# Kernel optimization log

Hardware: AMD Instinct MI355X
Metric: run time of the kernel (lower is better)

Reference implementation:

```python
import jax, jax.numpy as jnp
import numpy as np

B, S, HID, NH, NS = 2, 1024, 2048, 16, 8
D = HID // NH  # head_dim = 128


def setup_inputs() -> dict:
    key = jax.random.key(0)
    ks = jax.random.split(key, 8)
    inv = 1.0 / np.sqrt(HID)
    return {
        "hidden_states": jax.random.normal(ks[0], (B, S, HID), jnp.float32),
        "Wq": jax.random.normal(ks[1], (HID, HID), jnp.float32) * inv,
        "Wk": jax.random.normal(ks[2], (HID, HID), jnp.float32) * inv,
        "Wv": jax.random.normal(ks[3], (HID, HID), jnp.float32) * inv,
        "Wo": jax.random.normal(ks[4], (HID, HID), jnp.float32) * inv,
        "splat_positions": jax.random.normal(ks[5], (NH, NS, D), jnp.float32) * 0.02,
        "splat_directions": jax.random.normal(ks[6], (NH, NS, D), jnp.float32) * 0.02,
        "splat_log_scales": jnp.full((NH, NS), np.log(0.8), jnp.float32),
        "splat_log_amplitudes": jnp.full((NH, NS), -np.log(float(NS)), jnp.float32),
        "directional_strength": jnp.float32(0.3),
        "gsa_strength": jnp.float32(-6.0),
    }


def _affinities(tokens, positions, directions, scales, dir_strength):
    # tokens [B,NH,S,D]; positions/directions [NH,NS,D]; scales [NH,NS]
    tok_sq = jnp.sum(tokens * tokens, axis=-1)                       # [B,NH,S]
    pos_sq = jnp.sum(positions * positions, axis=-1)                 # [NH,NS]
    tp = jnp.einsum('bhsd,hnd->bhsn', tokens, positions)             # [B,NH,S,NS]
    dist2 = tok_sq[..., None] - 2.0 * tp + pos_sq[None, :, None, :]
    dist2 = jnp.maximum(dist2, 0.0)
    # signed projection of (token - position) onto unit direction
    proj = (jnp.einsum('bhsd,hnd->bhsn', tokens, directions)
            - jnp.sum(positions * directions, axis=-1)[None, :, None, :])
    perp2 = jnp.maximum(dist2 - proj * proj, 0.0)
    inv2s2 = (0.5 / (scales * scales))[None, :, None, :]
    radial = jnp.exp(-dist2 * inv2s2)
    directional = jnp.exp(-perp2 * inv2s2)
    return (1.0 - dir_strength) * radial + dir_strength * directional


def reference(hidden_states, Wq, Wk, Wv, Wo, splat_positions, splat_directions,
              splat_log_scales, splat_log_amplitudes, directional_strength, gsa_strength):
    b, s, hid = hidden_states.shape

    def heads(x):  # [B,S,HID] -> [B,NH,S,D]
        return x.reshape(b, s, NH, D).transpose(0, 2, 1, 3)

    q = heads(hidden_states @ Wq)
    k = heads(hidden_states @ Wk)
    v = heads(hidden_states @ Wv)

    # --- standard (original) attention path ---
    scores = jnp.einsum('bhqd,bhkd->bhqk', q, k) / jnp.sqrt(jnp.float32(D))
    attn = jax.nn.softmax(scores, axis=-1)
    std = jnp.einsum('bhqk,bhkd->bhqd', attn, v)
    std = std.transpose(0, 2, 1, 3).reshape(b, s, hid) @ Wo

    # --- directional GSA path ---
    eps = 1e-12
    positions = splat_positions / (jnp.linalg.norm(splat_positions, axis=-1, keepdims=True) + eps)
    positions = positions * (np.sqrt(D) * 0.3)
    directions = splat_directions / (jnp.linalg.norm(splat_directions, axis=-1, keepdims=True) + eps)
    scales = jnp.clip(jnp.exp(splat_log_scales), 0.3, 1.2)
    amplitudes = jax.nn.softmax(splat_log_amplitudes, axis=-1)
    ds = jax.nn.sigmoid(directional_strength)

    qa = _affinities(q, positions, directions, scales, ds)  # [B,NH,S,NS]
    ka = _affinities(k, positions, directions, scales, ds)  # [B,NH,S,NS]
    w = jnp.einsum('bhqn,hn,bhkn->bhqk', qa, amplitudes, ka)
    w = w / (jnp.sum(w, axis=-1, keepdims=True) + 1e-8)
    dgsa = jnp.einsum('bhqk,bhkd->bhqd', w, v)
    dgsa = dgsa.transpose(0, 2, 1, 3).reshape(b, s, hid) @ Wo

    gsa = jax.nn.sigmoid(gsa_strength)
    blend = jnp.minimum(0.05, gsa * 0.1)
    return (1.0 - blend) * std + blend * dgsa
```

## Files before the change

kernel.cpp:

```cpp
#include <hip/hip_runtime.h>
#include <math.h>

typedef __attribute__((ext_vector_type(8))) short bf16x8;
typedef __attribute__((ext_vector_type(4))) float f32x4;
typedef unsigned short ushort_t;

#define SQRT_D 11.313708498984761f
#define INV_SQRT_D 0.08838834764831845f

__device__ __forceinline__ unsigned short f2b(float f) {
    unsigned u = __float_as_uint(f);
    unsigned r = (u + 0x7fffu + ((u >> 16) & 1u)) >> 16;
    return (unsigned short)r;
}
__device__ __forceinline__ float b2f(unsigned short h) {
    return __uint_as_float(((unsigned)h) << 16);
}

__device__ __forceinline__ void async_copy16(const void* g, void* l) {
    __builtin_amdgcn_global_load_lds((const __attribute__((address_space(1))) void*)g,
                                     (__attribute__((address_space(3))) void*)l, 16, 0, 0);
}

__global__ __launch_bounds__(256) void prep(
    const float* __restrict__ X, const float* __restrict__ W0,
    const float* __restrict__ W1, const float* __restrict__ W2,
    const float* __restrict__ W3, const float* __restrict__ sp,
    const float* __restrict__ sd, const float* __restrict__ ls,
    const float* __restrict__ la, ushort_t* __restrict__ Xbf,
    ushort_t* __restrict__ WT4, float* __restrict__ posn,
    float* __restrict__ dirn, float* __restrict__ pos_sq,
    float* __restrict__ pdv, float* __restrict__ iv2s2,
    float* __restrict__ amp) {
    __shared__ float t[32][33];
    const int z = blockIdx.z;
    if (z < 4) {
        const float* W = (z == 0) ? W0 : (z == 1) ? W1 : (z == 2) ? W2 : W3;
        ushort_t* WT = WT4 + (size_t)z * 4194304;
        int tx = threadIdx.x & 31, ty = threadIdx.x >> 5;
        int bn = blockIdx.x * 32, bk = blockIdx.y * 32;
#pragma unroll
        for (int i = 0; i < 4; ++i)
            t[ty + i * 8][tx] = W[(size_t)(bk + ty + i * 8) * 2048 + bn + tx];
        __syncthreads();
#pragma unroll
        for (int i = 0; i < 4; ++i)
            WT[(size_t)(bn + ty + i * 8) * 2048 + bk + tx] = f2b(t[tx][ty + i * 8]);
        return;
    }
    {
        int bi = blockIdx.y * 64 + blockIdx.x;
        int i = (bi * 256 + threadIdx.x) * 4;
        float4 v = *(const float4*)(X + i);
        ushort4 o;
        o.x = f2b(v.x); o.y = f2b(v.y); o.z = f2b(v.z); o.w = f2b(v.w);
        *(ushort4*)(Xbf + i) = o;
    }
    if (blockIdx.x == 0 && blockIdx.y == 0 && threadIdx.x < 128) {
        int i = threadIdx.x;
        const float* p = sp + (size_t)i * 128;
        const float* d = sd + (size_t)i * 128;
        float np_ = 0.f, nd_ = 0.f;
        for (int k = 0; k < 128; ++k) { np_ += p[k] * p[k]; nd_ += d[k] * d[k]; }
        np_ = sqrtf(np_); nd_ = sqrtf(nd_);
        const float sc = 3.394112549695428f;
        float rp = sc / (np_ + 1e-12f);
        float rd = 1.f / (nd_ + 1e-12f);
        float psq = 0.f, pd_ = 0.f;
        for (int k = 0; k < 128; ++k) {
            float pn = p[k] * rp;
            float dn = d[k] * rd;
            posn[(size_t)i * 128 + k] = pn;
            dirn[(size_t)i * 128 + k] = dn;
            psq += pn * pn;
            pd_ += pn * dn;
        }
        pos_sq[i] = psq;
        pdv[i] = pd_;
        float s = expf(ls[i]);
        s = fminf(fmaxf(s, 0.3f), 1.2f);
        iv2s2[i] = 0.5f / (s * s);
        if ((i & 7) == 0) {
            int h = i >> 3;
            float mx = -INFINITY;
            for (int n = 0; n < 8; ++n) mx = fmaxf(mx, la[h * 8 + n]);
            float e[8]; float ssum = 0.f;
            for (int n = 0; n < 8; ++n) { e[n] = expf(la[h * 8 + n] - mx); ssum += e[n]; }
            for (int n = 0; n < 8; ++n) amp[h * 8 + n] = e[n] / ssum;
        }
    }
}


__global__ __launch_bounds__(256) void gemm_qkv(const ushort_t* __restrict__ A,
                                                const ushort_t* __restrict__ WT4,
                                                ushort_t* __restrict__ Qb,
                                                ushort_t* __restrict__ Kb,
                                                ushort_t* __restrict__ Vb,
                                                ushort_t* __restrict__ Vt) {
    __shared__ ushort_t As0[128 * 32], As1[128 * 32];
    __shared__ ushort_t Bs0[128 * 32], Bs1[128 * 32];
    const int tid = threadIdx.x, lane = tid & 63, wave = tid >> 6;
    const int l15 = lane & 15, quad = lane >> 4;
    const int wm = (wave >> 1) * 64, wn = (wave & 1) * 64;
    const int bm = blockIdx.x * 128;
    const int by = blockIdx.y, which = by >> 4, bn = (by & 15) * 128;
    const ushort_t* BT = WT4 + (size_t)which * 4194304;
    f32x4 acc[4][4] = {};
    const int off0 = tid * 16;
    const int row0 = tid >> 2;
    const int c0 = (tid & 3) ^ ((row0 + (row0 >> 2)) & 3);
    const ushort_t* ga = A + (size_t)(bm + row0) * 2048 + c0 * 8;
    const ushort_t* gb = BT + (size_t)(bn + row0) * 2048 + c0 * 8;
    const int rsw = (l15 + (l15 >> 2)) & 3;
#define STAGEG(ABUF, BBUF, k_)                                                 \
    {                                                                          \
        async_copy16(ga + (k_), (char*)(ABUF) + off0);                         \
        async_copy16(ga + (size_t)64 * 2048 + (k_), (char*)(ABUF) + off0 + 4096); \
        async_copy16(gb + (k_), (char*)(BBUF) + off0);                         \
        async_copy16(gb + (size_t)64 * 2048 + (k_), (char*)(BBUF) + off0 + 4096); \
    }
#define COMPUTEG(ABUF, BBUF)                                                   \
    {                                                                          \
        bf16x8 af[4], bfr[4];                                                  \
        _Pragma("unroll") for (int i = 0; i < 4; ++i)                          \
            af[i] = *(const bf16x8*)((const char*)(ABUF) + (wm + i * 16 + l15) * 64 + ((quad ^ rsw) << 4)); \
        _Pragma("unroll") for (int j = 0; j < 4; ++j)                          \
            bfr[j] = *(const bf16x8*)((const char*)(BBUF) + (wn + j * 16 + l15) * 64 + ((quad ^ rsw) << 4)); \
        _Pragma("unroll") for (int i = 0; i < 4; ++i)                          \
            _Pragma("unroll") for (int j = 0; j < 4; ++j)                      \
                acc[i][j] = __builtin_amdgcn_mfma_f32_16x16x32_bf16(af[i], bfr[j], acc[i][j], 0, 0, 0); \
    }
    STAGEG(As0, Bs0, 0);
    for (int k0 = 0; k0 < 2048; k0 += 64) {
        __syncthreads();
        STAGEG(As1, Bs1, k0 + 32);
        COMPUTEG(As0, Bs0);
        __syncthreads();
        if (k0 + 64 < 2048) STAGEG(As0, Bs0, k0 + 64);
        COMPUTEG(As1, Bs1);
    }
#undef STAGEG
#undef COMPUTEG
    ushort_t* Cb = (which == 0) ? Qb : ((which == 1) ? Kb : Vb);
    const bool dot = (which == 2);
    const float oscale = (which == 0) ? INV_SQRT_D : 1.f;
#pragma unroll
    for (int i = 0; i < 4; ++i) {
#pragma unroll
        for (int j = 0; j < 4; ++j) {
            int m0 = bm + wm + i * 16 + quad * 4;
            int n = bn + wn + j * 16 + l15;
            int b = m0 >> 10, s0 = m0 & 1023, h = n >> 7, d = n & 127;
            ushort4 pack;
            unsigned short* pp = (unsigned short*)&pack;
#pragma unroll
            for (int r = 0; r < 4; ++r) {
                unsigned short bv = f2b(acc[i][j][r] * oscale);
                pp[r] = bv;
                Cb[((size_t)((b << 4) | h) * 1024 + (s0 + r)) * 128 + d] = bv;
            }
            if (dot) *(ushort4*)(Vt + ((size_t)((b << 4) | h) * 128 + d) * 1024 + s0) = pack;
        }
    }
}

__global__ __launch_bounds__(256) void gemm_out(const ushort_t* __restrict__ A,
                                                const ushort_t* __restrict__ BT,
                                                float* __restrict__ Cf) {
    __shared__ ushort_t As0[128 * 32], As1[128 * 32];
    __shared__ ushort_t Bs0[128 * 32], Bs1[128 * 32];
    const int tid = threadIdx.x, lane = tid & 63, wave = tid >> 6;
    const int l15 = lane & 15, quad = lane >> 4;
    const int wm = (wave >> 1) * 64, wn = (wave & 1) * 64;
    const int bm = blockIdx.x * 128, bn = blockIdx.y * 128;
    f32x4 acc[4][4] = {};
    const int off0 = tid * 16;
    const int row0 = tid >> 2;
    const int c0 = (tid & 3) ^ ((row0 + (row0 >> 2)) & 3);
    const ushort_t* ga = A + (size_t)(bm + row0) * 2048 + c0 * 8;
    const ushort_t* gb = BT + (size_t)(bn + row0) * 2048 + c0 * 8;
    const int rsw = (l15 + (l15 >> 2)) & 3;
#define STAGEO(ABUF, BBUF, k_)                                                 \
    {                                                                          \
        async_copy16(ga + (k_), (char*)(ABUF) + off0);                         \
        async_copy16(ga + (size_t)64 * 2048 + (k_), (char*)(ABUF) + off0 + 4096); \
        async_copy16(gb + (k_), (char*)(BBUF) + off0);                         \
        async_copy16(gb + (size_t)64 * 2048 + (k_), (char*)(BBUF) + off0 + 4096); \
    }
#define COMPUTEO(ABUF, BBUF)                                                   \
    {                                                                          \
        bf16x8 af[4], bfr[4];                                                  \
        _Pragma("unroll") for (int i = 0; i < 4; ++i)                          \
            af[i] = *(const bf16x8*)((const char*)(ABUF) + (wm + i * 16 + l15) * 64 + ((quad ^ rsw) << 4)); \
        _Pragma("unroll") for (int j = 0; j < 4; ++j)                          \
            bfr[j] = *(const bf16x8*)((const char*)(BBUF) + (wn + j * 16 + l15) * 64 + ((quad ^ rsw) << 4)); \
        _Pragma("unroll") for (int i = 0; i < 4; ++i)                          \
            _Pragma("unroll") for (int j = 0; j < 4; ++j)                      \
                acc[i][j] = __builtin_amdgcn_mfma_f32_16x16x32_bf16(af[i], bfr[j], acc[i][j], 0, 0, 0); \
    }
    STAGEO(As0, Bs0, 0);
    for (int k0 = 0; k0 < 2048; k0 += 64) {
        __syncthreads();
        STAGEO(As1, Bs1, k0 + 32);
        COMPUTEO(As0, Bs0);
        __syncthreads();
        if (k0 + 64 < 2048) STAGEO(As0, Bs0, k0 + 64);
        COMPUTEO(As1, Bs1);
    }
#undef STAGEO
#undef COMPUTEO
#pragma unroll
    for (int i = 0; i < 4; ++i)
#pragma unroll
        for (int j = 0; j < 4; ++j)
#pragma unroll
            for (int r = 0; r < 4; ++r) {
                int m = bm + wm + i * 16 + quad * 4 + r;
                int n = bn + wn + j * 16 + l15;
                Cf[(size_t)m * 2048 + n] = acc[i][j][r];
            }
}

__global__ __launch_bounds__(256) void affinity_q(
    const ushort_t* __restrict__ Q,
    const float* __restrict__ posn, const float* __restrict__ dirn,
    const float* __restrict__ pos_sq, const float* __restrict__ pdv,
    const float* __restrict__ iv2s2, const float* __restrict__ ds_in,
    float* __restrict__ qa) {
    int gid = blockIdx.x * 256 + threadIdx.x;
    int n = gid & 7;
    int t = gid >> 3;
    const ushort_t* T = Q + (size_t)t * 128;
    int h = (t >> 10) & 15;
    const float* P = posn + (size_t)(h * 8 + n) * 128;
    const float* Dr = dirn + (size_t)(h * 8 + n) * 128;
    float tsq = 0.f, tp = 0.f, td = 0.f;
#pragma unroll
    for (int d = 0; d < 128; d += 8) {
        uint4 raw = *(const uint4*)(T + d);
        float tv[8];
        tv[0] = __uint_as_float(raw.x << 16); tv[1] = __uint_as_float(raw.x & 0xffff0000u);
        tv[2] = __uint_as_float(raw.y << 16); tv[3] = __uint_as_float(raw.y & 0xffff0000u);
        tv[4] = __uint_as_float(raw.z << 16); tv[5] = __uint_as_float(raw.z & 0xffff0000u);
        tv[6] = __uint_as_float(raw.w << 16); tv[7] = __uint_as_float(raw.w & 0xffff0000u);
        float4 p0 = *(const float4*)(P + d), p1 = *(const float4*)(P + d + 4);
        float4 d0 = *(const float4*)(Dr + d), d1 = *(const float4*)(Dr + d + 4);
        tsq += tv[0]*tv[0]+tv[1]*tv[1]+tv[2]*tv[2]+tv[3]*tv[3]+tv[4]*tv[4]+tv[5]*tv[5]+tv[6]*tv[6]+tv[7]*tv[7];
        tp  += tv[0]*p0.x+tv[1]*p0.y+tv[2]*p0.z+tv[3]*p0.w+tv[4]*p1.x+tv[5]*p1.y+tv[6]*p1.z+tv[7]*p1.w;
        td  += tv[0]*d0.x+tv[1]*d0.y+tv[2]*d0.z+tv[3]*d0.w+tv[4]*d1.x+tv[5]*d1.y+tv[6]*d1.z+tv[7]*d1.w;
    }
    const float fs = SQRT_D;
    tsq *= fs * fs; tp *= fs; td *= fs;
    float dist2 = fmaxf(tsq - 2.f * tp + pos_sq[h * 8 + n], 0.f);
    float proj = td - pdv[h * 8 + n];
    float perp2 = fmaxf(dist2 - proj * proj, 0.f);
    float iv = iv2s2[h * 8 + n];
    float dsv = 1.f / (1.f + __expf(-ds_in[0]));
    float aff = (1.f - dsv) * __expf(-dist2 * iv) + dsv * __expf(-perp2 * iv);
    qa[(size_t)t * 8 + n] = aff;
}

__global__ __launch_bounds__(128) void kv_s1_part(
    const ushort_t* __restrict__ K, const ushort_t* __restrict__ V,
    const float* __restrict__ posn, const float* __restrict__ dirn,
    const float* __restrict__ pos_sq, const float* __restrict__ pdv,
    const float* __restrict__ iv2s2, const float* __restrict__ ds_in,
    float* __restrict__ KVp, float* __restrict__ S1p) {
    __shared__ float kas[64][8];
    int bh = blockIdx.x, sc = blockIdx.y;
    int tid = threadIdx.x;
    int h = bh & 15;
    if (tid < 64) {
        const ushort_t* T = K + ((size_t)bh * 1024 + sc * 64 + tid) * 128;
        float tsq = 0.f, tp[8] = {}, td[8] = {};
        for (int d = 0; d < 128; d += 4) {
            uint2 raw = *(const uint2*)(T + d);
            float t0 = __uint_as_float(raw.x << 16), t1 = __uint_as_float(raw.x & 0xffff0000u);
            float t2 = __uint_as_float(raw.y << 16), t3 = __uint_as_float(raw.y & 0xffff0000u);
            tsq += t0 * t0 + t1 * t1 + t2 * t2 + t3 * t3;
#pragma unroll
            for (int n = 0; n < 8; ++n) {
                const float* P = posn + (size_t)(h * 8 + n) * 128 + d;
                const float* Dr = dirn + (size_t)(h * 8 + n) * 128 + d;
                tp[n] += t0 * P[0] + t1 * P[1] + t2 * P[2] + t3 * P[3];
                td[n] += t0 * Dr[0] + t1 * Dr[1] + t2 * Dr[2] + t3 * Dr[3];
            }
        }
        float dsv = 1.f / (1.f + __expf(-ds_in[0]));
#pragma unroll
        for (int n = 0; n < 8; ++n) {
            float dist2 = fmaxf(tsq - 2.f * tp[n] + pos_sq[h * 8 + n], 0.f);
            float proj = td[n] - pdv[h * 8 + n];
            float perp2 = fmaxf(dist2 - proj * proj, 0.f);
            float iv = iv2s2[h * 8 + n];
            kas[tid][n] = (1.f - dsv) * __expf(-dist2 * iv) + dsv * __expf(-perp2 * iv);
        }
    }
    __syncthreads();
    int d = tid;
    const ushort_t* VB = V + ((size_t)bh * 1024 + sc * 64) * 128;
    float acc[8] = {};
#pragma unroll 4
    for (int s = 0; s < 64; ++s) {
        float vd = b2f(VB[(size_t)s * 128 + d]);
#pragma unroll
        for (int n = 0; n < 8; ++n) acc[n] += kas[s][n] * vd;
    }
#pragma unroll
    for (int n = 0; n < 8; ++n) KVp[(((size_t)bh * 8 + n) * 16 + sc) * 128 + d] = acc[n];
    __shared__ float s1p[128];
    {
        int n = d >> 4, chunk = d & 15;
        float p = 0.f;
        for (int s = chunk * 4; s < chunk * 4 + 4; ++s) p += kas[s][n];
        s1p[d] = p;
    }
    __syncthreads();
    if (d < 8) {
        float t = 0.f;
        for (int c = 0; c < 16; ++c) t += s1p[(d << 4) + c];
        S1p[((size_t)bh * 8 + d) * 16 + sc] = t;
    }
}

__global__ __launch_bounds__(256) void flash_blend(
    const ushort_t* __restrict__ Qg, const ushort_t* __restrict__ Kg,
    const ushort_t* __restrict__ Vtg,
    const float* __restrict__ qa, const float* __restrict__ amp,
    const float* __restrict__ S1p, const float* __restrict__ KVp,
    const float* __restrict__ gstr, ushort_t* __restrict__ blended) {
    __shared__ ushort_t Ks0[64 * 128], Ks1[64 * 128];
    __shared__ ushort_t Vt0[128 * 64], Vt1[128 * 64];
    __shared__ ushort_t Ps[4][16 * 72];
    __shared__ float KVs[8 * 128];
    __shared__ float S1s[8];
    const int tid = threadIdx.x, lane = tid & 63, wave = tid >> 6;
    const int l15 = lane & 15, quad = lane >> 4;
    const int bh = blockIdx.y, qt = blockIdx.x;

    const ushort_t* Qrow = Qg + ((size_t)(bh * 1024 + qt * 64 + wave * 16 + l15)) * 128 + quad * 8;
    bf16x8 aq[4];
#pragma unroll
    for (int k4 = 0; k4 < 4; ++k4) aq[k4] = *(const bf16x8*)(Qrow + k4 * 32);

    {
        int n = tid >> 5, d = (tid & 31) * 4;
        f32x4 kv = {};
#pragma unroll
        for (int sc = 0; sc < 16; ++sc)
            kv += *(const f32x4*)(KVp + (((size_t)bh * 8 + n) * 16 + sc) * 128 + d);
        *(f32x4*)(KVs + tid * 4) = kv;
    }
    if (tid < 8) {
        float s = 0.f;
#pragma unroll
        for (int sc = 0; sc < 16; ++sc) s += S1p[((size_t)bh * 8 + tid) * 16 + sc];
        S1s[tid] = s;
    }

    const ushort_t* Kbase = Kg + (size_t)bh * 131072;
    const ushort_t* Vbase = Vtg + (size_t)bh * 131072;

#define STAGE(KBUF, VBUF, kt_)                                                        \
    {                                                                                 \
        _Pragma("unroll") for (int i_ = 0; i_ < 4; ++i_) {                            \
            int off_ = tid * 16 + i_ * 4096;                                          \
            int kr_ = off_ >> 8, kp_ = (off_ >> 4) & 15;                              \
            async_copy16(Kbase + (size_t)(kt_)*8192 + kr_ * 128 + ((kp_ ^ (kr_ & 15)) << 3), \
                         (char*)(KBUF) + off_);                                       \
            int vd_ = off_ >> 7, vp_ = (off_ >> 4) & 7;                               \
            async_copy16(Vbase + (size_t)vd_ * 1024 + (kt_)*64 + ((vp_ ^ (vd_ & 7)) << 3), \
                         (char*)(VBUF) + off_);                                       \
        }                                                                             \
    }
#define FLASH_STEP(KBUF, VBUF)                                                        \
    {                                                                                 \
        f32x4 sc[4] = {};                                                             \
        _Pragma("unroll") for (int k4 = 0; k4 < 4; ++k4) {                            \
            _Pragma("unroll") for (int t = 0; t < 4; ++t) {                           \
                bf16x8 bk = *(const bf16x8*)((const char*)(KBUF) +                    \
                                             ((t * 16 + l15) << 8) + (((k4 * 4 + quad) ^ l15) << 4)); \
                sc[t] = __builtin_amdgcn_mfma_f32_16x16x32_bf16(aq[k4], bk, sc[t], 0, 0, 0); \
            }                                                                         \
        }                                                                             \
        _Pragma("unroll") for (int t = 0; t < 4; ++t) {                               \
            _Pragma("unroll") for (int r = 0; r < 4; ++r) {                           \
                float p = __expf(sc[t][r]);                                           \
                l_i[r] += p;                                                          \
                Pw[(quad * 4 + r) * 72 + t * 16 + l15] = f2b(p);                      \
            }                                                                         \
        }                                                                             \
        bf16x8 ap0 = *(const bf16x8*)((const char*)Pw + (l15 * 72 + quad * 8) * 2);   \
        bf16x8 ap1 = *(const bf16x8*)((const char*)Pw + (l15 * 72 + 32 + quad * 8) * 2); \
        _Pragma("unroll") for (int j = 0; j < 8; ++j) {                               \
            bf16x8 bv0 = *(const bf16x8*)((const char*)(VBUF) +                       \
                                          ((j * 16 + l15) << 7) + (((quad) ^ (l15 & 7)) << 4)); \
            bf16x8 bv1 = *(const bf16x8*)((const char*)(VBUF) +                       \
                                          ((j * 16 + l15) << 7) + (((4 + quad) ^ (l15 & 7)) << 4)); \
            o[j] = __builtin_amdgcn_mfma_f32_16x16x32_bf16(ap0, bv0, o[j], 0, 0, 0);  \
            o[j] = __builtin_amdgcn_mfma_f32_16x16x32_bf16(ap1, bv1, o[j], 0, 0, 0);  \
        }                                                                             \
    }

    STAGE(Ks0, Vt0, 0);

    f32x4 o[8] = {};
    float l_i[4] = {};
    ushort_t* Pw = &Ps[wave][0];

    for (int kt = 0; kt < 16; kt += 2) {
        __syncthreads();
        STAGE(Ks1, Vt1, kt + 1);
        FLASH_STEP(Ks0, Vt0);
        __syncthreads();
        if (kt + 2 < 16) STAGE(Ks0, Vt0, kt + 2);
        FLASH_STEP(Ks1, Vt1);
    }
#undef STAGE
#undef FLASH_STEP
#pragma unroll
    for (int r = 0; r < 4; ++r) {
        float l = l_i[r];
        l += __shfl_xor(l, 1);
        l += __shfl_xor(l, 2);
        l += __shfl_xor(l, 4);
        l += __shfl_xor(l, 8);
        l_i[r] = l;
    }
    float gsa = 1.f / (1.f + __expf(-gstr[0]));
    float blend = fminf(0.05f, gsa * 0.1f);
    int b = bh >> 4, h = bh & 15;
#pragma unroll
    for (int r = 0; r < 4; ++r) {
        int q = qt * 64 + wave * 16 + quad * 4 + r;
        const float* qaRow = qa + ((size_t)bh * 1024 + q) * 8;
        float qam[8], Z = 0.f;
#pragma unroll
        for (int n = 0; n < 8; ++n) {
            qam[n] = qaRow[n] * amp[h * 8 + n];
            Z += qam[n] * S1s[n];
        }
        float invZ = 1.f / (Z + 1e-8f);
        float invl = 1.f / l_i[r];
        ushort_t* outp = blended + ((size_t)(b * 1024 + q)) * 2048 + h * 128;
#pragma unroll
        for (int j = 0; j < 8; ++j) {
            int d = j * 16 + l15;
            float dg = 0.f;
#pragma unroll
            for (int n = 0; n < 8; ++n) dg += qam[n] * KVs[n * 128 + d];
            float v = (1.f - blend) * (o[j][r] * invl) + blend * (dg * invZ);
            outp[d] = f2b(v);
        }
    }
}

extern "C" void kernel_launch(void* const* d_in, const int* in_sizes, int n_in,
                              void* d_out, int out_size, void* d_ws, size_t ws_size,
                              hipStream_t stream) {
    const float* X = (const float*)d_in[0];
    const float* Wq = (const float*)d_in[1];
    const float* Wk = (const float*)d_in[2];
    const float* Wv = (const float*)d_in[3];
    const float* Wo = (const float*)d_in[4];
    const float* sp = (const float*)d_in[5];
    const float* sd = (const float*)d_in[6];
    const float* ls = (const float*)d_in[7];
    const float* la = (const float*)d_in[8];
    const float* dstr = (const float*)d_in[9];
    const float* gstr = (const float*)d_in[10];

    char* base = (char*)d_ws;
    ushort_t* WT4 = (ushort_t*)base;      base += 33554432;
    ushort_t* Xbf = (ushort_t*)base;      base += 8388608;
    ushort_t* blended = Xbf;
    ushort_t* Qbf = (ushort_t*)base;      base += 8388608;
    ushort_t* Kbf = (ushort_t*)base;      base += 8388608;
    ushort_t* Vbf = (ushort_t*)base;      base += 8388608;
    ushort_t* Vtb = (ushort_t*)base;      base += 8388608;
    float* qaw = (float*)base;            base += 1048576;
    float* posn = (float*)base;           base += 65536;
    float* dirn = (float*)base;           base += 65536;
    float* pos_sq = (float*)base;         base += 512;
    float* pdv = (float*)base;            base += 512;
    float* iv2s2 = (float*)base;          base += 512;
    float* ampw = (float*)base;           base += 512;
    float* S1p = (float*)base;            base += 16384;
    float* KVp = (float*)base;            base += 2097152;

    prep<<<dim3(64, 64, 5), 256, 0, stream>>>(X, Wq, Wk, Wv, Wo, sp, sd, ls, la,
                                              Xbf, WT4, posn, dirn, pos_sq, pdv, iv2s2, ampw);
    gemm_qkv<<<dim3(16, 48), 256, 0, stream>>>(Xbf, WT4, Qbf, Kbf, Vbf, Vtb);
    affinity_q<<<1024, 256, 0, stream>>>(Qbf, posn, dirn, pos_sq, pdv, iv2s2, dstr, qaw);
    kv_s1_part<<<dim3(32, 16), 128, 0, stream>>>(Kbf, Vbf, posn, dirn, pos_sq, pdv, iv2s2,
                                                 dstr, KVp, S1p);
    flash_blend<<<dim3(16, 32), 256, 0, stream>>>(Qbf, Kbf, Vtb, qaw, ampw, S1p, KVp,
                                                  gstr, blended);
    gemm_out<<<dim3(16, 16), 256, 0, stream>>>(blended, WT4 + 12582912, (float*)d_out);
}
```

Before: 328.7 us.

## Read K/V directly from global in flash kernel, halve block size

Removes the double-buffered LDS staging of K and Vt tiles with async copies and barriers; each wave now loads MFMA operands for K and Vt straight from global memory, relying on L1/L2 caching. The query tile shrinks to 32 rows with 128-thread blocks, doubling the grid to 1024 blocks. This cuts LDS usage and synchronization to raise occupancy, at the cost of redundant, less-coalesced global reads of K/V shared across waves.

```diff
diff --git a/kernel.cpp b/kernel.cpp
--- a/kernel.cpp
+++ b/kernel.cpp
@@ -324,33 +324,35 @@
     }
 }
 
-__global__ __launch_bounds__(256) void flash_blend(
+__global__ __launch_bounds__(128) void flash_blend(
     const ushort_t* __restrict__ Qg, const ushort_t* __restrict__ Kg,
     const ushort_t* __restrict__ Vtg,
     const float* __restrict__ qa, const float* __restrict__ amp,
     const float* __restrict__ S1p, const float* __restrict__ KVp,
     const float* __restrict__ gstr, ushort_t* __restrict__ blended) {
-    __shared__ ushort_t Ks0[64 * 128], Ks1[64 * 128];
-    __shared__ ushort_t Vt0[128 * 64], Vt1[128 * 64];
-    __shared__ ushort_t Ps[4][16 * 72];
+    __shared__ ushort_t Ps[2][16 * 72];
     __shared__ float KVs[8 * 128];
     __shared__ float S1s[8];
     const int tid = threadIdx.x, lane = tid & 63, wave = tid >> 6;
     const int l15 = lane & 15, quad = lane >> 4;
     const int bh = blockIdx.y, qt = blockIdx.x;
 
-    const ushort_t* Qrow = Qg + ((size_t)(bh * 1024 + qt * 64 + wave * 16 + l15)) * 128 + quad * 8;
+    const ushort_t* Qrow = Qg + ((size_t)(bh * 1024 + qt * 32 + wave * 16 + l15)) * 128 + quad * 8;
     bf16x8 aq[4];
 #pragma unroll
     for (int k4 = 0; k4 < 4; ++k4) aq[k4] = *(const bf16x8*)(Qrow + k4 * 32);
 
     {
-        int n = tid >> 5, d = (tid & 31) * 4;
-        f32x4 kv = {};
-#pragma unroll
-        for (int sc = 0; sc < 16; ++sc)
-            kv += *(const f32x4*)(KVp + (((size_t)bh * 8 + n) * 16 + sc) * 128 + d);
-        *(f32x4*)(KVs + tid * 4) = kv;
+        int n = tid >> 4, d0 = (tid & 15) * 8;
+        f32x4 kv0 = {}, kv1 = {};
+#pragma unroll
+        for (int sc = 0; sc < 16; ++sc) {
+            const float* src = KVp + (((size_t)bh * 8 + n) * 16 + sc) * 128 + d0;
+            kv0 += *(const f32x4*)(src);
+            kv1 += *(const f32x4*)(src + 4);
+        }
+        *(f32x4*)(KVs + n * 128 + d0) = kv0;
+        *(f32x4*)(KVs + n * 128 + d0 + 4) = kv1;
     }
     if (tid < 8) {
         float s = 0.f;
@@ -361,64 +363,43 @@
 
     const ushort_t* Kbase = Kg + (size_t)bh * 131072;
     const ushort_t* Vbase = Vtg + (size_t)bh * 131072;
-
-#define STAGE(KBUF, VBUF, kt_)                                                        \
-    {                                                                                 \
-        _Pragma("unroll") for (int i_ = 0; i_ < 4; ++i_) {                            \
-            int off_ = tid * 16 + i_ * 4096;                                          \
-            int kr_ = off_ >> 8, kp_ = (off_ >> 4) & 15;                              \
-            async_copy16(Kbase + (size_t)(kt_)*8192 + kr_ * 128 + ((kp_ ^ (kr_ & 15)) << 3), \
-                         (char*)(KBUF) + off_);                                       \
-            int vd_ = off_ >> 7, vp_ = (off_ >> 4) & 7;                               \
-            async_copy16(Vbase + (size_t)vd_ * 1024 + (kt_)*64 + ((vp_ ^ (vd_ & 7)) << 3), \
-                         (char*)(VBUF) + off_);                                       \
-        }                                                                             \
-    }
-#define FLASH_STEP(KBUF, VBUF)                                                        \
-    {                                                                                 \
-        f32x4 sc[4] = {};                                                             \
-        _Pragma("unroll") for (int k4 = 0; k4 < 4; ++k4) {                            \
-            _Pragma("unroll") for (int t = 0; t < 4; ++t) {                           \
-                bf16x8 bk = *(const bf16x8*)((const char*)(KBUF) +                    \
-                                             ((t * 16 + l15) << 8) + (((k4 * 4 + quad) ^ l15) << 4)); \
-                sc[t] = __builtin_amdgcn_mfma_f32_16x16x32_bf16(aq[k4], bk, sc[t], 0, 0, 0); \
-            }                                                                         \
-        }                                                                             \
-        _Pragma("unroll") for (int t = 0; t < 4; ++t) {                               \
-            _Pragma("unroll") for (int r = 0; r < 4; ++r) {                           \
-                float p = __expf(sc[t][r]);                                           \
-                l_i[r] += p;                                                          \
-                Pw[(quad * 4 + r) * 72 + t * 16 + l15] = f2b(p);                      \
-            }                                                                         \
-        }                                                                             \
-        bf16x8 ap0 = *(const bf16x8*)((const char*)Pw + (l15 * 72 + quad * 8) * 2);   \
-        bf16x8 ap1 = *(const bf16x8*)((const char*)Pw + (l15 * 72 + 32 + quad * 8) * 2); \
-        _Pragma("unroll") for (int j = 0; j < 8; ++j) {                               \
-            bf16x8 bv0 = *(const bf16x8*)((const char*)(VBUF) +                       \
-                                          ((j * 16 + l15) << 7) + (((quad) ^ (l15 & 7)) << 4)); \
-            bf16x8 bv1 = *(const bf16x8*)((const char*)(VBUF) +                       \
-                                          ((j * 16 + l15) << 7) + (((4 + quad) ^ (l15 & 7)) << 4)); \
-            o[j] = __builtin_amdgcn_mfma_f32_16x16x32_bf16(ap0, bv0, o[j], 0, 0, 0);  \
-            o[j] = __builtin_amdgcn_mfma_f32_16x16x32_bf16(ap1, bv1, o[j], 0, 0, 0);  \
-        }                                                                             \
-    }
-
-    STAGE(Ks0, Vt0, 0);
 
     f32x4 o[8] = {};
     float l_i[4] = {};
     ushort_t* Pw = &Ps[wave][0];
 
-    for (int kt = 0; kt < 16; kt += 2) {
-        __syncthreads();
-        STAGE(Ks1, Vt1, kt + 1);
-        FLASH_STEP(Ks0, Vt0);
-        __syncthreads();
-        if (kt + 2 < 16) STAGE(Ks0, Vt0, kt + 2);
-        FLASH_STEP(Ks1, Vt1);
-    }
-#undef STAGE
-#undef FLASH_STEP
+    for (int kt = 0; kt < 16; ++kt) {
+        const ushort_t* Kt = Kbase + kt * 8192;
+        const ushort_t* Vt_ = Vbase + kt * 64;
+        f32x4 sc[4] = {};
+#pragma unroll
+        for (int k4 = 0; k4 < 4; ++k4) {
+#pragma unroll
+            for (int t = 0; t < 4; ++t) {
+                bf16x8 bk = *(const bf16x8*)(Kt + (t * 16 + l15) * 128 + (k4 * 4 + quad) * 8);
+                sc[t] = __builtin_amdgcn_mfma_f32_16x16x32_bf16(aq[k4], bk, sc[t], 0, 0, 0);
+            }
+        }
+#pragma unroll
+        for (int t = 0; t < 4; ++t) {
+#pragma unroll
+            for (int r = 0; r < 4; ++r) {
+                float p = __expf(sc[t][r]);
+                l_i[r] += p;
+                Pw[(quad * 4 + r) * 72 + t * 16 + l15] = f2b(p);
+            }
+        }
+        bf16x8 ap0 = *(const bf16x8*)((const char*)Pw + (l15 * 72 + quad * 8) * 2);
+        bf16x8 ap1 = *(const bf16x8*)((const char*)Pw + (l15 * 72 + 32 + quad * 8) * 2);
+#pragma unroll
+        for (int j = 0; j < 8; ++j) {
+            bf16x8 bv0 = *(const bf16x8*)(Vt_ + (size_t)(j * 16 + l15) * 1024 + quad * 8);
+            bf16x8 bv1 = *(const bf16x8*)(Vt_ + (size_t)(j * 16 + l15) * 1024 + 32 + quad * 8);
+            o[j] = __builtin_amdgcn_mfma_f32_16x16x32_bf16(ap0, bv0, o[j], 0, 0, 0);
+            o[j] = __builtin_amdgcn_mfma_f32_16x16x32_bf16(ap1, bv1, o[j], 0, 0, 0);
+        }
+    }
+
 #pragma unroll
     for (int r = 0; r < 4; ++r) {
         float l = l_i[r];
@@ -428,12 +409,13 @@
         l += __shfl_xor(l, 8);
         l_i[r] = l;
     }
+    __syncthreads();
     float gsa = 1.f / (1.f + __expf(-gstr[0]));
     float blend = fminf(0.05f, gsa * 0.1f);
     int b = bh >> 4, h = bh & 15;
 #pragma unroll
     for (int r = 0; r < 4; ++r) {
-        int q = qt * 64 + wave * 16 + quad * 4 + r;
+        int q = qt * 32 + wave * 16 + quad * 4 + r;
         const float* qaRow = qa + ((size_t)bh * 1024 + q) * 8;
         float qam[8], Z = 0.f;
 #pragma unroll
@@ -495,7 +477,7 @@
     affinity_q<<<1024, 256, 0, stream>>>(Qbf, posn, dirn, pos_sq, pdv, iv2s2, dstr, qaw);
     kv_s1_part<<<dim3(32, 16), 128, 0, stream>>>(Kbf, Vbf, posn, dirn, pos_sq, pdv, iv2s2,
                                                  dstr, KVp, S1p);
-    flash_blend<<<dim3(16, 32), 256, 0, stream>>>(Qbf, Kbf, Vtb, qaw, ampw, S1p, KVp,
+    flash_blend<<<dim3(32, 32), 128, 0, stream>>>(Qbf, Kbf, Vtb, qaw, ampw, S1p, KVp,
                                                   gstr, blended);
     gemm_out<<<dim3(16, 16), 256, 0, stream>>>(blended, WT4 + 12582912, (float*)d_out);
 }
```

After: 427.9 us. 30.2% more time.
